# Optimization experiments

Measured on AMD Instinct MI355X. Metric: run time of the kernel, lower is better.

## Reference

```python
import jax, jax.numpy as jnp
import numpy as np

ALPHA = 0.2  # LeakyReLU negative slope
NEG_INF = -9e15


def setup_inputs() -> dict:
    key = jax.random.key(0)
    k1, k2, k3, k4 = jax.random.split(key, 4)
    N, IN_F, OUT_F, H = 8192, 256, 128, 2
    HD = OUT_F // H
    h = jax.random.normal(k1, (N, IN_F), dtype=jnp.float32)
    adj = jax.random.randint(k2, (N, N), 0, 2, dtype=jnp.int32)
    # xavier_uniform with gain=1.414
    g = 1.414
    limW = g * np.sqrt(6.0 / (IN_F + HD))
    W = jax.random.uniform(k3, (H, IN_F, HD), jnp.float32, -limW, limW)
    lima = g * np.sqrt(6.0 / (2 * HD + 1))
    a = jax.random.uniform(k4, (H, 2 * HD, 1), jnp.float32, -lima, lima)
    return {"h": h, "adj": adj, "W": W, "a": a}


def reference(h, adj, W, a):
    # Wh: (H, N, HD)
    Wh = jnp.einsum('ni,hid->hnd', h, W)
    HD = W.shape[-1]
    a1 = a[:, :HD, 0]   # (H, HD) -> applied to Wh_i
    a2 = a[:, HD:, 0]   # (H, HD) -> applied to Wh_j
    # a . [Wh_i || Wh_j] == a1.Wh_i + a2.Wh_j ; avoids the (N,N,2HD) tensor
    f1 = jnp.einsum('hnd,hd->hn', Wh, a1)  # (H, N)
    f2 = jnp.einsum('hnd,hd->hn', Wh, a2)  # (H, N)
    e = jax.nn.leaky_relu(f1[:, :, None] + f2[:, None, :], ALPHA)  # (H, N, N)
    mask = (adj > 0)[None, :, :]
    e = jnp.where(mask, e, NEG_INF)
    attention = jax.nn.softmax(e, axis=-1)  # (H, N, N)
    # dropout is identity in eval mode
    h_prime = jnp.einsum('hnm,hmd->hnd', attention, Wh)  # (H, N, HD)
    N = h.shape[0]
    h_prime = jnp.transpose(h_prime, (1, 0, 2)).reshape(N, -1)  # concat heads
    return jax.nn.elu(h_prime)
```

## Files before the change

kernel.cpp:

```cpp
#include <hip/hip_runtime.h>
#include <hip/hip_bf16.h>
#include <stdint.h>

#define N_NODES 8192
#define IN_F    256
#define HD      64
#define NH      2
#define MS      8
#define NT      ((N_NODES / MS) / 64)
#define ALPHA   0.2f

typedef __attribute__((ext_vector_type(8))) short bf16x8s;
typedef __attribute__((ext_vector_type(4))) float f32x4;

#define OFF_U      0
#define OFF_WFRAG  4096
#define OFF_F1     69632
#define OFF_F2     135168
#define OFF_F2MAX  200704
#define OFF_G2     200960
#define OFF_WHB    332032
#define OFF_OP     2429184
#define OFF_LP     35983616

__device__ __forceinline__ unsigned short f2bf(float x) {
  union { float f; uint32_t u; } c; c.f = x;
  uint32_t r = c.u + 0x7FFFu + ((c.u >> 16) & 1u);
  return (unsigned short)(r >> 16);
}
__device__ __forceinline__ short f2bfs(float x) {
  __hip_bfloat16 b = __float2bfloat16(x);
  return __builtin_bit_cast(short, b);
}

__global__ void gat_prep_kernel(const float* __restrict__ W, const float* __restrict__ a,
                                float* __restrict__ u, unsigned short* __restrict__ wfrag)
{
  int idx = blockIdx.x * 256 + threadIdx.x;
  if (idx < 32768) {
    int j = idx & 7, lane = (idx >> 3) & 63, ks = (idx >> 9) & 7, Dt = idx >> 12;
    int k  = ks * 32 + ((lane >> 4) << 3) + j;
    int dp = Dt * 16 + (lane & 15);
    int hh = dp >> 6, d = dp & 63;
    wfrag[idx] = f2bf(W[(size_t)(hh * IN_F + k) * HD + d]);
  } else if (idx < 32768 + NH * 2 * IN_F) {
    int i2 = idx - 32768;
    int i = i2 & 255, v = (i2 >> 8) & 1, h = i2 >> 9;
    const float* Wp = W + (size_t)(h * IN_F + i) * HD;
    const float* ap = a + h * 2 * HD + v * HD;
    float s = 0.f;
    for (int d = 0; d < HD; ++d) s += Wp[d] * ap[d];
    u[(h * 2 + v) * IN_F + i] = s;
  }
}

__global__ __launch_bounds__(256) void gat_f12_kernel(const float* __restrict__ hmat,
    const float* __restrict__ u, float* __restrict__ f1, float* __restrict__ f2,
    float2* __restrict__ g2)
{
  int n = blockIdx.x * 4 + (threadIdx.x >> 6);
  int l = threadIdx.x & 63;
  float4 hv = *(const float4*)(hmat + (size_t)n * IN_F + l * 4);
  float s[4];
#pragma unroll
  for (int q = 0; q < 4; ++q) {
    float4 uv = *(const float4*)(u + q * IN_F + l * 4);
    s[q] = hv.x * uv.x + hv.y * uv.y + hv.z * uv.z + hv.w * uv.w;
  }
#pragma unroll
  for (int off = 1; off < 64; off <<= 1) {
#pragma unroll
    for (int q = 0; q < 4; ++q) s[q] += __shfl_xor(s[q], off);
  }
  if (l == 0) {
    f1[n] = s[0];           f2[n] = s[1];
    f1[N_NODES + n] = s[2]; f2[N_NODES + n] = s[3];
    g2[n]           = make_float2(__expf(s[1]), __expf(ALPHA * s[1]));
    g2[N_NODES + n] = make_float2(__expf(s[3]), __expf(ALPHA * s[3]));
  }
}

__global__ void gat_f2max_kernel(const float* __restrict__ f2, float* __restrict__ f2m)
{
  int h = blockIdx.x;
  float m = -1e30f;
  for (int i = threadIdx.x; i < N_NODES; i += 256) m = fmaxf(m, f2[h * N_NODES + i]);
#pragma unroll
  for (int off = 1; off < 64; off <<= 1) m = fmaxf(m, __shfl_xor(m, off));
  __shared__ float red[4];
  if ((threadIdx.x & 63) == 0) red[threadIdx.x >> 6] = m;
  __syncthreads();
  if (threadIdx.x == 0) f2m[h] = fmaxf(fmaxf(red[0], red[1]), fmaxf(red[2], red[3]));
}

__global__ __launch_bounds__(256) void gat_wh_kernel(const float* __restrict__ hmat,
    const unsigned short* __restrict__ wfrag, unsigned short* __restrict__ whb)
{
  int tid = threadIdx.x;
  int w = tid >> 6, l = tid & 63;
  int n0 = blockIdx.x * 64;
  int row = n0 + w * 16 + (l & 15);
  f32x4 acc[8] = {};
#pragma unroll
  for (int ks = 0; ks < 8; ++ks) {
    const float* ap = hmat + (size_t)row * IN_F + ks * 32 + ((l >> 4) << 3);
    float av[8];
    *(float4*)&av[0] = *(const float4*)ap;
    *(float4*)&av[4] = *(const float4*)(ap + 4);
    bf16x8s af;
#pragma unroll
    for (int j = 0; j < 8; ++j) af[j] = f2bfs(av[j]);
#pragma unroll
    for (int Dt = 0; Dt < 8; ++Dt) {
      bf16x8s bfv = *(const bf16x8s*)(wfrag + ((size_t)(Dt * 8 + ks) * 64 + l) * 8);
      acc[Dt] = __builtin_amdgcn_mfma_f32_16x16x32_bf16(af, bfv, acc[Dt], 0, 0, 0);
    }
  }
  int Tm = blockIdx.x;
  int s  = w >> 1;
  int lb = ((w & 1) * 2 + ((l >> 4) >> 1)) * 16 + (l & 15);
  int jh = (l >> 4) & 1;
#pragma unroll
  for (int Dt = 0; Dt < 8; ++Dt) {
    int hh = Dt >> 2, D = Dt & 3;
    ushort4 pk;
    pk.x = f2bf(acc[Dt][0]); pk.y = f2bf(acc[Dt][1]);
    pk.z = f2bf(acc[Dt][2]); pk.w = f2bf(acc[Dt][3]);
    size_t off = ((((size_t)(hh * 128 + Tm) * 2 + s) * 4 + D) * 64 + lb) * 8 + jh * 4;
    *(ushort4*)(whb + off) = pk;
  }
}

#define LOADADJ(d0, d1, d2, d3, p, base) \
  d0 = *(const int4*)((p) + (base));      d1 = *(const int4*)((p) + (base) + 4); \
  d2 = *(const int4*)((p) + (base) + 32); d3 = *(const int4*)((p) + (base) + 36);

__global__ __launch_bounds__(256, 2) void gat_attn_kernel(
    const int* __restrict__ adj, const unsigned short* __restrict__ whb,
    const float* __restrict__ f1, const float2* __restrict__ g2,
    const float* __restrict__ f2max, float* __restrict__ Opart, float* __restrict__ Lpart)
{
  int bx = blockIdx.x;
  int split = bx & (MS - 1);
  int T = bx >> 3;
  int tid = threadIdx.x;
  int w = tid >> 6, l = tid & 63;
  int n0 = T * 128;
  int rbase = n0 + w * 16 + (l & 15);
  int mbase = split * (N_NODES / MS);
  int koff = (l >> 4) << 3;

  float E1[NH][2], Ea[NH][2];
#pragma unroll
  for (int h = 0; h < NH; ++h)
#pragma unroll
    for (int rg = 0; rg < 2; ++rg) {
      float f1v = f1[h * N_NODES + rbase + rg * 64];
      float tm  = f1v + f2max[h];
      float mrow = fmaxf(tm, ALPHA * tm);
      E1[h][rg] = __expf(f1v - mrow);
      Ea[h][rg] = __expf(ALPHA * f1v - mrow);
    }

  __shared__ float4 gl[2][512];
  __shared__ uint4  wbuf[1024];

  {
    const float4* s0 = (const float4*)(g2 + mbase);
    const float4* s1 = (const float4*)(g2 + N_NODES + mbase);
    gl[0][tid] = s0[tid]; gl[0][tid + 256] = s0[tid + 256];
    gl[1][tid] = s1[tid]; gl[1][tid + 256] = s1[tid + 256];
  }

  const int* adjr0 = adj + (size_t)rbase * N_NODES + mbase + koff;
  const int* adjr1 = adjr0 + (size_t)64 * N_NODES;
  const uint4* ws0 = (const uint4*)(whb + ((size_t)(mbase >> 6)) * 4096);
  const uint4* ws1 = (const uint4*)(whb + ((size_t)(128 + (mbase >> 6))) * 4096);

  int4 cA0, cA1, cA2, cA3, cB0, cB1, cB2, cB3;
  int4 nA0, nA1, nA2, nA3, nB0, nB1, nB2, nB3;
  LOADADJ(cA0, cA1, cA2, cA3, adjr0, 0);
  LOADADJ(cB0, cB1, cB2, cB3, adjr1, 0);
  LOADADJ(nA0, nA1, nA2, nA3, adjr0, 64);
  LOADADJ(nB0, nB1, nB2, nB3, adjr1, 64);
  uint4 rw0 = ws0[tid], rw1 = ws0[tid + 256];
  uint4 rw2 = ws1[tid], rw3 = ws1[tid + 256];

  f32x4 acc[NH][2][4] = {};
  float lsum[NH][2] = {};

  for (int mt = 0; mt < NT; ++mt) {
    __syncthreads();
    wbuf[tid]       = rw0; wbuf[tid + 256] = rw1;
    wbuf[tid + 512] = rw2; wbuf[tid + 768] = rw3;
    if (mt + 1 < NT) {
      const uint4* wp0 = ws0 + (size_t)(mt + 1) * 512;
      const uint4* wp1 = ws1 + (size_t)(mt + 1) * 512;
      rw0 = wp0[tid]; rw1 = wp0[tid + 256];
      rw2 = wp1[tid]; rw3 = wp1[tid + 256];
    }
    __syncthreads();

    int ajA[16], ajB[16];
    *(int4*)&ajA[0] = cA0; *(int4*)&ajA[4]  = cA1;
    *(int4*)&ajA[8] = cA2; *(int4*)&ajA[12] = cA3;
    *(int4*)&ajB[0] = cB0; *(int4*)&ajB[4]  = cB1;
    *(int4*)&ajB[8] = cB2; *(int4*)&ajB[12] = cB3;

#pragma unroll
    for (int h = 0; h < NH; ++h) {
      bf16x8s afA[2], afB[2];
#pragma unroll
      for (int s = 0; s < 2; ++s) {
        const float4* gp = &gl[h][(mt * 64 + s * 32 + koff) >> 1];
        float psA = 0.f, psB = 0.f;
#pragma unroll
        for (int k = 0; k < 4; ++k) {
          float4 gv = gp[k];
          float m1x = E1[h][0] * gv.x, max_ = Ea[h][0] * gv.y;
          float pA0 = (ajA[s * 8 + 2 * k]     > 0) ? fmaxf(m1x, max_) : 0.f;
          float m1z = E1[h][0] * gv.z, maz = Ea[h][0] * gv.w;
          float pA1 = (ajA[s * 8 + 2 * k + 1] > 0) ? fmaxf(m1z, maz) : 0.f;
          float n1x = E1[h][1] * gv.x, nax = Ea[h][1] * gv.y;
          float pB0 = (ajB[s * 8 + 2 * k]     > 0) ? fmaxf(n1x, nax) : 0.f;
          float n1z = E1[h][1] * gv.z, naz = Ea[h][1] * gv.w;
          float pB1 = (ajB[s * 8 + 2 * k + 1] > 0) ? fmaxf(n1z, naz) : 0.f;
          psA += pA0 + pA1;  psB += pB0 + pB1;
          afA[s][2 * k] = f2bfs(pA0); afA[s][2 * k + 1] = f2bfs(pA1);
          afB[s][2 * k] = f2bfs(pB0); afB[s][2 * k + 1] = f2bfs(pB1);
        }
        lsum[h][0] += psA; lsum[h][1] += psB;
      }
      const unsigned short* lb = (const unsigned short*)wbuf + h * 4096;
#pragma unroll
      for (int s = 0; s < 2; ++s)
#pragma unroll
        for (int D = 0; D < 4; ++D) {
          bf16x8s bfv = *(const bf16x8s*)&lb[(s * 4 + D) * 512 + l * 8];
          acc[h][0][D] = __builtin_amdgcn_mfma_f32_16x16x32_bf16(afA[s], bfv, acc[h][0][D], 0, 0, 0);
          acc[h][1][D] = __builtin_amdgcn_mfma_f32_16x16x32_bf16(afB[s], bfv, acc[h][1][D], 0, 0, 0);
        }
    }

    cA0 = nA0; cA1 = nA1; cA2 = nA2; cA3 = nA3;
    cB0 = nB0; cB1 = nB1; cB2 = nB2; cB3 = nB3;
    if (mt + 2 < NT) {
      LOADADJ(nA0, nA1, nA2, nA3, adjr0, (mt + 2) * 64);
      LOADADJ(nB0, nB1, nB2, nB3, adjr1, (mt + 2) * 64);
    }
  }

#pragma unroll
  for (int h = 0; h < NH; ++h)
#pragma unroll
    for (int rg = 0; rg < 2; ++rg) {
      float ls = lsum[h][rg];
      ls += __shfl_xor(ls, 16);
      ls += __shfl_xor(ls, 32);
      if (l < 16) Lpart[((size_t)(split * NH + h) << 13) + n0 + rg * 64 + w * 16 + l] = ls;
      float* op = Opart + (size_t)(split * NH + h) * N_NODES * HD;
#pragma unroll
      for (int D = 0; D < 4; ++D)
#pragma unroll
        for (int r = 0; r < 4; ++r) {
          int orow = n0 + rg * 64 + w * 16 + ((l >> 4) << 2) + r;
          op[(size_t)orow * HD + D * 16 + (l & 15)] = acc[h][rg][D][r];
        }
    }
}

__global__ __launch_bounds__(256) void gat_final_kernel(const float* __restrict__ Opart,
    const float* __restrict__ Lpart, float* __restrict__ out)
{
  int idx = blockIdx.x * 256 + threadIdx.x;
  int n = idx >> 7, c = idx & 127;
  int h = c >> 6, d = c & 63;
  float v = 0.f, ls = 0.f;
#pragma unroll
  for (int sp = 0; sp < MS; ++sp) {
    v  += Opart[((size_t)(sp * NH + h) * N_NODES + n) * HD + d];
    ls += Lpart[(size_t)(sp * NH + h) * N_NODES + n];
  }
  float r = v / fmaxf(ls, 1e-30f);
  out[idx] = (r > 0.f) ? r : (__expf(r) - 1.f);
}

extern "C" void kernel_launch(void* const* d_in, const int* in_sizes, int n_in,
                              void* d_out, int out_size, void* d_ws, size_t ws_size,
                              hipStream_t stream)
{
  const float* hmat = (const float*)d_in[0];
  const int*   adj  = (const int*)d_in[1];
  const float* W    = (const float*)d_in[2];
  const float* a    = (const float*)d_in[3];
  float* out = (float*)d_out;
  char* ws = (char*)d_ws;

  float* u             = (float*)(ws + OFF_U);
  unsigned short* wfrg = (unsigned short*)(ws + OFF_WFRAG);
  float* f1            = (float*)(ws + OFF_F1);
  float* f2            = (float*)(ws + OFF_F2);
  float* f2m           = (float*)(ws + OFF_F2MAX);
  float2* g2           = (float2*)(ws + OFF_G2);
  unsigned short* whb  = (unsigned short*)(ws + OFF_WHB);
  float* Opart         = (float*)(ws + OFF_OP);
  float* Lpart         = (float*)(ws + OFF_LP);

  gat_prep_kernel <<<132, 256, 0, stream>>>(W, a, u, wfrg);
  gat_f12_kernel  <<<N_NODES / 4, 256, 0, stream>>>(hmat, u, f1, f2, g2);
  gat_f2max_kernel<<<NH, 256, 0, stream>>>(f2, f2m);
  gat_wh_kernel   <<<N_NODES / 64, 256, 0, stream>>>(hmat, wfrg, whb);
  gat_attn_kernel <<<64 * MS, 256, 0, stream>>>(adj, whb, f1, g2, f2m, Opart, Lpart);
  gat_final_kernel<<<out_size / 256, 256, 0, stream>>>(Opart, Lpart, out);
}
```

Baseline: 109.4 us.

## Pack adjacency into bitmask in a pre-pass and consume bits in attention

```diff
diff --git a/kernel.cpp b/kernel.cpp
--- a/kernel.cpp
+++ b/kernel.cpp
@@ -22,6 +22,7 @@
 #define OFF_WHB    332032
 #define OFF_OP     2429184
 #define OFF_LP     35983616
+#define OFF_MB     36507648
 
 __device__ __forceinline__ unsigned short f2bf(float x) {
   union { float f; uint32_t u; } c; c.f = x;
@@ -31,6 +32,27 @@
 __device__ __forceinline__ short f2bfs(float x) {
   __hip_bfloat16 b = __float2bfloat16(x);
   return __builtin_bit_cast(short, b);
+}
+
+__global__ __launch_bounds__(256) void gat_pack_kernel(const int* __restrict__ adj,
+    unsigned long long* __restrict__ mbits)
+{
+  int w = threadIdx.x >> 6, l = threadIdx.x & 63;
+  int r = blockIdx.x * 4 + w;
+  const int4* src = (const int4*)(adj + (size_t)r * N_NODES) + l;
+  unsigned long long* dst = mbits + (size_t)r * 128;
+#pragma unroll 2
+  for (int c = 0; c < 32; ++c) {
+    int4 v = src[c * 64];
+    unsigned long long b0 = __ballot(v.x > 0);
+    unsigned long long b1 = __ballot(v.y > 0);
+    unsigned long long b2 = __ballot(v.z > 0);
+    unsigned long long b3 = __ballot(v.w > 0);
+    if (l == 0) {
+      *(ulonglong2*)(dst + c * 4)     = make_ulonglong2(b0, b1);
+      *(ulonglong2*)(dst + c * 4 + 2) = make_ulonglong2(b2, b3);
+    }
+  }
 }
 
 __global__ void gat_prep_kernel(const float* __restrict__ W, const float* __restrict__ a,
@@ -131,12 +153,8 @@
   }
 }
 
-#define LOADADJ(d0, d1, d2, d3, p, base) \
-  d0 = *(const int4*)((p) + (base));      d1 = *(const int4*)((p) + (base) + 4); \
-  d2 = *(const int4*)((p) + (base) + 32); d3 = *(const int4*)((p) + (base) + 36);
-
 __global__ __launch_bounds__(256, 2) void gat_attn_kernel(
-    const int* __restrict__ adj, const unsigned short* __restrict__ whb,
+    const unsigned long long* __restrict__ mbits, const unsigned short* __restrict__ whb,
     const float* __restrict__ f1, const float2* __restrict__ g2,
     const float* __restrict__ f2max, float* __restrict__ Opart, float* __restrict__ Lpart)
 {
@@ -172,17 +190,15 @@
     gl[1][tid] = s1[tid]; gl[1][tid + 256] = s1[tid + 256];
   }
 
-  const int* adjr0 = adj + (size_t)rbase * N_NODES + mbase + koff;
-  const int* adjr1 = adjr0 + (size_t)64 * N_NODES;
+  int cb0 = mbase >> 8;
+  const ulonglong2* mp0 = (const ulonglong2*)mbits + (size_t)rbase * 64 + cb0 * 2;
+  const ulonglong2* mp1 = mp0 + (size_t)64 * 64;
+
   const uint4* ws0 = (const uint4*)(whb + ((size_t)(mbase >> 6)) * 4096);
   const uint4* ws1 = (const uint4*)(whb + ((size_t)(128 + (mbase >> 6))) * 4096);
 
-  int4 cA0, cA1, cA2, cA3, cB0, cB1, cB2, cB3;
-  int4 nA0, nA1, nA2, nA3, nB0, nB1, nB2, nB3;
-  LOADADJ(cA0, cA1, cA2, cA3, adjr0, 0);
-  LOADADJ(cB0, cB1, cB2, cB3, adjr1, 0);
-  LOADADJ(nA0, nA1, nA2, nA3, adjr0, 64);
-  LOADADJ(nB0, nB1, nB2, nB3, adjr1, 64);
+  ulonglong2 cmA0 = mp0[0], cmA1 = mp0[1], cmB0 = mp1[0], cmB1 = mp1[1];
+  ulonglong2 nmA0 = mp0[2], nmA1 = mp0[3], nmB0 = mp1[2], nmB1 = mp1[3];
   uint4 rw0 = ws0[tid], rw1 = ws0[tid + 256];
   uint4 rw2 = ws1[tid], rw3 = ws1[tid + 256];
 
@@ -199,54 +215,62 @@
       rw0 = wp0[tid]; rw1 = wp0[tid + 256];
       rw2 = wp1[tid]; rw3 = wp1[tid + 256];
     }
+    if (mt && (mt & 3) == 0) {
+      cmA0 = nmA0; cmA1 = nmA1; cmB0 = nmB0; cmB1 = nmB1;
+      int cb = (mt >> 2) + 1;
+      if (cb < NT / 4) {
+        nmA0 = mp0[cb * 2]; nmA1 = mp0[cb * 2 + 1];
+        nmB0 = mp1[cb * 2]; nmB1 = mp1[cb * 2 + 1];
+      }
+    }
     __syncthreads();
 
-    int ajA[16], ajB[16];
-    *(int4*)&ajA[0] = cA0; *(int4*)&ajA[4]  = cA1;
-    *(int4*)&ajA[8] = cA2; *(int4*)&ajA[12] = cA3;
-    *(int4*)&ajB[0] = cB0; *(int4*)&ajB[4]  = cB1;
-    *(int4*)&ajB[8] = cB2; *(int4*)&ajB[12] = cB3;
-
-#pragma unroll
-    for (int h = 0; h < NH; ++h) {
-      bf16x8s afA[2], afB[2];
-#pragma unroll
-      for (int s = 0; s < 2; ++s) {
+    int shbase = ((mt & 3) << 4) + ((l >> 4) << 1);
+    bf16x8s afA[NH][2], afB[NH][2];
+#pragma unroll
+    for (int s = 0; s < 2; ++s) {
+      int sh = shbase + s * 8;
+      uint32_t t0 = (uint32_t)(cmA0.x >> sh), t1 = (uint32_t)(cmA0.y >> sh);
+      uint32_t t2 = (uint32_t)(cmA1.x >> sh), t3 = (uint32_t)(cmA1.y >> sh);
+      uint32_t u0 = (uint32_t)(cmB0.x >> sh), u1 = (uint32_t)(cmB0.y >> sh);
+      uint32_t u2 = (uint32_t)(cmB1.x >> sh), u3 = (uint32_t)(cmB1.y >> sh);
+#pragma unroll
+      for (int h = 0; h < NH; ++h) {
         const float4* gp = &gl[h][(mt * 64 + s * 32 + koff) >> 1];
         float psA = 0.f, psB = 0.f;
 #pragma unroll
         for (int k = 0; k < 4; ++k) {
           float4 gv = gp[k];
-          float m1x = E1[h][0] * gv.x, max_ = Ea[h][0] * gv.y;
-          float pA0 = (ajA[s * 8 + 2 * k]     > 0) ? fmaxf(m1x, max_) : 0.f;
-          float m1z = E1[h][0] * gv.z, maz = Ea[h][0] * gv.w;
-          float pA1 = (ajA[s * 8 + 2 * k + 1] > 0) ? fmaxf(m1z, maz) : 0.f;
-          float n1x = E1[h][1] * gv.x, nax = Ea[h][1] * gv.y;
-          float pB0 = (ajB[s * 8 + 2 * k]     > 0) ? fmaxf(n1x, nax) : 0.f;
-          float n1z = E1[h][1] * gv.z, naz = Ea[h][1] * gv.w;
-          float pB1 = (ajB[s * 8 + 2 * k + 1] > 0) ? fmaxf(n1z, naz) : 0.f;
+          uint32_t txA = (k & 1) ? t2 : t0, tyA = (k & 1) ? t3 : t1;
+          uint32_t txB = (k & 1) ? u2 : u0, tyB = (k & 1) ? u3 : u1;
+          int kb = k >> 1;
+          float vA0 = fmaxf(E1[h][0] * gv.x, Ea[h][0] * gv.y);
+          float vA1 = fmaxf(E1[h][0] * gv.z, Ea[h][0] * gv.w);
+          float vB0 = fmaxf(E1[h][1] * gv.x, Ea[h][1] * gv.y);
+          float vB1 = fmaxf(E1[h][1] * gv.z, Ea[h][1] * gv.w);
+          float pA0 = ((txA >> kb) & 1) ? vA0 : 0.f;
+          float pA1 = ((tyA >> kb) & 1) ? vA1 : 0.f;
+          float pB0 = ((txB >> kb) & 1) ? vB0 : 0.f;
+          float pB1 = ((tyB >> kb) & 1) ? vB1 : 0.f;
           psA += pA0 + pA1;  psB += pB0 + pB1;
-          afA[s][2 * k] = f2bfs(pA0); afA[s][2 * k + 1] = f2bfs(pA1);
-          afB[s][2 * k] = f2bfs(pB0); afB[s][2 * k + 1] = f2bfs(pB1);
+          afA[h][s][2 * k] = f2bfs(pA0); afA[h][s][2 * k + 1] = f2bfs(pA1);
+          afB[h][s][2 * k] = f2bfs(pB0); afB[h][s][2 * k + 1] = f2bfs(pB1);
         }
         lsum[h][0] += psA; lsum[h][1] += psB;
       }
+    }
+
+#pragma unroll
+    for (int h = 0; h < NH; ++h) {
       const unsigned short* lb = (const unsigned short*)wbuf + h * 4096;
 #pragma unroll
       for (int s = 0; s < 2; ++s)
 #pragma unroll
         for (int D = 0; D < 4; ++D) {
           bf16x8s bfv = *(const bf16x8s*)&lb[(s * 4 + D) * 512 + l * 8];
-          acc[h][0][D] = __builtin_amdgcn_mfma_f32_16x16x32_bf16(afA[s], bfv, acc[h][0][D], 0, 0, 0);
-          acc[h][1][D] = __builtin_amdgcn_mfma_f32_16x16x32_bf16(afB[s], bfv, acc[h][1][D], 0, 0, 0);
+          acc[h][0][D] = __builtin_amdgcn_mfma_f32_16x16x32_bf16(afA[h][s], bfv, acc[h][0][D], 0, 0, 0);
+          acc[h][1][D] = __builtin_amdgcn_mfma_f32_16x16x32_bf16(afB[h][s], bfv, acc[h][1][D], 0, 0, 0);
         }
-    }
-
-    cA0 = nA0; cA1 = nA1; cA2 = nA2; cA3 = nA3;
-    cB0 = nB0; cB1 = nB1; cB2 = nB2; cB3 = nB3;
-    if (mt + 2 < NT) {
-      LOADADJ(nA0, nA1, nA2, nA3, adjr0, (mt + 2) * 64);
-      LOADADJ(nB0, nB1, nB2, nB3, adjr1, (mt + 2) * 64);
     }
   }
 
@@ -305,11 +329,13 @@
   unsigned short* whb  = (unsigned short*)(ws + OFF_WHB);
   float* Opart         = (float*)(ws + OFF_OP);
   float* Lpart         = (float*)(ws + OFF_LP);
-
+  unsigned long long* mbits = (unsigned long long*)(ws + OFF_MB);
+
+  gat_pack_kernel <<<N_NODES / 4, 256, 0, stream>>>(adj, mbits);
   gat_prep_kernel <<<132, 256, 0, stream>>>(W, a, u, wfrg);
   gat_f12_kernel  <<<N_NODES / 4, 256, 0, stream>>>(hmat, u, f1, f2, g2);
   gat_f2max_kernel<<<NH, 256, 0, stream>>>(f2, f2m);
   gat_wh_kernel   <<<N_NODES / 64, 256, 0, stream>>>(hmat, wfrg, whb);
-  gat_attn_kernel <<<64 * MS, 256, 0, stream>>>(adj, whb, f1, g2, f2m, Opart, Lpart);
+  gat_attn_kernel <<<64 * MS, 256, 0, stream>>>(mbits, whb, f1, g2, f2m, Opart, Lpart);
   gat_final_kernel<<<out_size / 256, 256, 0, stream>>>(Opart, Lpart, out);
 }
```

Measured after the change: 132.6 us. 21.2% more time.
